# Performance work log

Measured on AMD Instinct MI355X. Metric: run time of the kernel, lower is better.

Reference implementation:

```python
import jax, jax.numpy as jnp
import numpy as np

N = 20000   # nodes
E = 320000  # edges
F0 = 32     # num_features
H = 8       # GAT heads
G = 64      # graphs in batch


def setup_inputs() -> dict:
    key = jax.random.key(0)
    ks = jax.random.split(key, 16)
    def p(k, shape, s=0.05):
        return jax.random.normal(k, shape, jnp.float32) * s
    d = {}
    d['x'] = jax.random.normal(ks[0], (N, F0), jnp.float32)
    d['edge_index'] = jax.random.randint(ks[1], (2, E), 0, N, dtype=jnp.int32)
    d['edge_weights'] = jax.random.uniform(ks[2], (E,), jnp.float32)
    d['batch'] = jnp.sort(jax.random.randint(ks[3], (N,), 0, G, dtype=jnp.int32))
    # GATConv(32 -> 32, heads=8)
    d['W_gat'] = p(ks[4], (F0, H * F0)); d['att_src'] = p(ks[5], (H, F0))
    d['att_dst'] = p(ks[6], (H, F0));    d['b_gat'] = jnp.zeros((H * F0,), jnp.float32)
    # residual Linear(256 -> 1024) (widened so the residual add is shape-consistent)
    d['W_res'] = p(ks[7], (H * F0, 1024)); d['b_res'] = jnp.zeros((1024,), jnp.float32)
    # GCNConv(256 -> 512) + BN1
    d['W2'] = p(ks[8], (H * F0, 512)); d['b2'] = jnp.zeros((512,), jnp.float32)
    d['g1'] = jnp.ones((512,), jnp.float32); d['be1'] = jnp.zeros((512,), jnp.float32)
    d['m1'] = jnp.zeros((512,), jnp.float32); d['v1'] = jnp.ones((512,), jnp.float32)
    # GCNConv(512 -> 1024) + BN2
    d['W3'] = p(ks[9], (512, 1024)); d['b3'] = jnp.zeros((1024,), jnp.float32)
    d['g2'] = jnp.ones((1024,), jnp.float32); d['be2'] = jnp.zeros((1024,), jnp.float32)
    d['m2'] = jnp.zeros((1024,), jnp.float32); d['v2'] = jnp.ones((1024,), jnp.float32)
    # head
    d['Wf1'] = p(ks[10], (1024, 256)); d['bf1'] = jnp.zeros((256,), jnp.float32)
    d['Wf2'] = p(ks[11], (256, 2));    d['bf2'] = jnp.zeros((2,), jnp.float32)
    return d


def _add_self_loops(edge_index, edge_weight, n):
    loop = jnp.arange(n, dtype=edge_index.dtype)
    ei = jnp.concatenate([edge_index, jnp.stack([loop, loop])], axis=1)
    ew = jnp.concatenate([edge_weight, jnp.ones((n,), edge_weight.dtype)])
    return ei, ew


def _gat(x, edge_index, W, att_src, att_dst, b, n):
    # PyG GATConv, concat=True, eval (attention dropout off). Self-loops already added.
    src, dst = edge_index[0], edge_index[1]
    h = (x @ W).reshape(n, H, -1)                    # [N,H,C]
    a_s = jnp.einsum('nhc,hc->nh', h, att_src)        # [N,H]
    a_d = jnp.einsum('nhc,hc->nh', h, att_dst)
    e = jax.nn.leaky_relu(a_s[src] + a_d[dst], 0.2)   # [E,H]
    m = jax.ops.segment_max(e, dst, num_segments=n)   # softmax over incoming edges
    ex = jnp.exp(e - m[dst])
    s = jax.ops.segment_sum(ex, dst, num_segments=n)
    alpha = ex / s[dst]
    out = jax.ops.segment_sum(h[src] * alpha[:, :, None], dst, num_segments=n)
    return out.reshape(n, -1) + b                     # [N,H*C]


def _gcn(x, edge_index, w, W, b, n):
    # PyG GCNConv with symmetric normalization; self-loops (weight 1) already added.
    src, dst = edge_index[0], edge_index[1]
    deg = jax.ops.segment_sum(w, dst, num_segments=n)
    dinv = jnp.where(deg > 0, jax.lax.rsqrt(jnp.maximum(deg, 1e-12)), 0.0)
    norm = dinv[src] * w * dinv[dst]                  # [E]
    h = x @ W                                         # transform first (cheaper)
    return jax.ops.segment_sum(h[src] * norm[:, None], dst, num_segments=n) + b


def _bn(x, g, b, m, v):
    return g * (x - m) * jax.lax.rsqrt(v + 1e-5) + b


def reference(x, edge_index, edge_weights, batch, W_gat, att_src, att_dst, b_gat,
              W_res, b_res, W2, b2, g1, be1, m1, v1, W3, b3, g2, be2, m2, v2,
              Wf1, bf1, Wf2, bf2):
    n = x.shape[0]
    ei, ew = _add_self_loops(edge_index, edge_weights, n)
    h = jax.nn.relu(_gat(x, ei, W_gat, att_src, att_dst, b_gat, n))   # [N,256]
    res = h @ W_res + b_res                                           # [N,1024]
    h = _gcn(h, ei, ew, W2, b2, n)                                    # [N,512]
    h = jax.nn.relu(_bn(h, g1, be1, m1, v1))
    h = _gcn(h, ei, ew, W3, b3, n)                                    # [N,1024]
    h = jax.nn.relu(_bn(h, g2, be2, m2, v2))
    h = h + res
    pooled = jax.ops.segment_max(h, batch, num_segments=G)            # global max pool [G,1024]
    z = jax.nn.relu(pooled @ Wf1 + bf1)                               # dropout is eval no-op
    return z @ Wf2 + bf2                                              # [G,2]
```

## Files before the change

kernel.cpp:

```cpp
#include <hip/hip_runtime.h>
#include <hip/hip_bf16.h>

#define NN 20000
#define EE 320000
#define GG 64
#define EN (EE + NN)
#define MT 157
#define SB 79

typedef float f32x4 __attribute__((ext_vector_type(4)));
typedef __bf16 bf16x4 __attribute__((ext_vector_type(4)));
typedef __bf16 bf16x8 __attribute__((ext_vector_type(8)));

__device__ __forceinline__ void gl_lds16(const void* g, void* l) {
    __builtin_amdgcn_global_load_lds((const __attribute__((address_space(1))) void*)g,
                                     (__attribute__((address_space(3))) void*)l, 16, 0, 0);
}

__global__ void sentinel_kernel(float* out, int n) {
    int i = blockIdx.x * 256 + threadIdx.x;
    if (i < n) out[i] = 12345.0f;
}

__global__ void init_kernel(int* deg_cnt, float* deg_w, int* fill, float* pooled) {
    int i = blockIdx.x * 256 + threadIdx.x;
    if (i < NN) { deg_cnt[i] = 1; deg_w[i] = 1.0f; fill[i] = 0; }
    if (i < GG * 1024) pooled[i] = -INFINITY;
}

__global__ void deg_kernel(const int* __restrict__ ei, const float* __restrict__ ew,
                           int* deg_cnt, float* deg_w) {
    int e = blockIdx.x * 256 + threadIdx.x;
    if (e >= EE) return;
    int dst = ei[EE + e];
    atomicAdd(&deg_cnt[dst], 1);
    atomicAdd(&deg_w[dst], ew[e]);
}

__global__ __launch_bounds__(256) void scan_blocks(const int* __restrict__ deg_cnt, int* __restrict__ bsum) {
    __shared__ int red[256];
    int tid = threadIdx.x, i = blockIdx.x * 256 + tid;
    red[tid] = (i < NN) ? deg_cnt[i] : 0;
    __syncthreads();
    for (int s = 128; s > 0; s >>= 1) { if (tid < s) red[tid] += red[tid + s]; __syncthreads(); }
    if (tid == 0) bsum[blockIdx.x] = red[0];
}

__global__ __launch_bounds__(256) void scan_write(const int* __restrict__ deg_cnt,
                                                  const int* __restrict__ bsum, int* __restrict__ rowptr) {
    __shared__ int sc[256];
    __shared__ int red[256];
    int tid = threadIdx.x, b = blockIdx.x, i = b * 256 + tid;
    red[tid] = (tid < b && tid < SB) ? bsum[tid] : 0;
    __syncthreads();
    for (int s = 128; s > 0; s >>= 1) { if (tid < s) red[tid] += red[tid + s]; __syncthreads(); }
    int boff = red[0];
    __syncthreads();
    int v = (i < NN) ? deg_cnt[i] : 0;
    sc[tid] = v;
    __syncthreads();
    for (int ofs = 1; ofs < 256; ofs <<= 1) {
        int t = (tid >= ofs) ? sc[tid - ofs] : 0;
        __syncthreads();
        sc[tid] += t;
        __syncthreads();
    }
    if (i < NN) rowptr[i] = boff + sc[tid] - v;
    if (b == SB - 1 && tid == 255) rowptr[NN] = boff + sc[255];
}

__global__ void fill_kernel(const int* __restrict__ ei, const float* __restrict__ ew,
                            const float* __restrict__ deg_w, const int* __restrict__ rowptr,
                            int* fill, int2* __restrict__ csre) {
    int e = blockIdx.x * 256 + threadIdx.x;
    if (e >= EN) return;
    int src, dst; float w;
    if (e < EE) { src = ei[e]; dst = ei[EE + e]; w = ew[e]; }
    else        { src = dst = e - EE; w = 1.0f; }
    int pos = atomicAdd(&fill[dst], 1);
    int slot = rowptr[dst] + pos;
    float norm = rsqrtf(deg_w[src]) * w * rsqrtf(deg_w[dst]);
    csre[slot] = make_int2(src, __float_as_int(norm));
}

__global__ __launch_bounds__(256) void convert_all(
    const float* __restrict__ W2, const float* __restrict__ W3, const float* __restrict__ Wres,
    __bf16* __restrict__ W2t, __bf16* __restrict__ W3t, __bf16* __restrict__ Wrt)
{
    __shared__ float tile[64][65];
    int b = blockIdx.x;
    const float* W; __bf16* Wt; int K, N, bx, by;
    if (b < 32)       { W = W2;   Wt = W2t; K = 256; N = 512;  int bb = b;       bx = bb & 7;  by = bb >> 3; }
    else if (b < 160) { W = W3;   Wt = W3t; K = 512; N = 1024; int bb = b - 32;  bx = bb & 15; by = bb >> 4; }
    else              { W = Wres; Wt = Wrt; K = 256; N = 1024; int bb = b - 160; bx = bb & 15; by = bb >> 4; }
    int kb = by * 64, nb = bx * 64;
    int tx = threadIdx.x & 63, ty = threadIdx.x >> 6;
#pragma unroll
    for (int i = ty; i < 64; i += 4)
        tile[i][tx] = W[(size_t)(kb + i) * N + nb + tx];
    __syncthreads();
#pragma unroll
    for (int i = ty; i < 64; i += 4)
        Wt[(size_t)(nb + i) * K + kb + tx] = (__bf16)tile[tx][i];
}


__global__ __launch_bounds__(256) void a_compute(
    const float* __restrict__ x, const float* __restrict__ W,
    const float* __restrict__ att_s, const float* __restrict__ att_d,
    float* __restrict__ a_s, float* __restrict__ a_d)
{
    __shared__ float wss[8][32], wsd[8][32];
    __shared__ float xs[32][33];
    int tid = threadIdx.x;
    {
        int h = tid >> 5, k = tid & 31;
        float s = 0.f, d = 0.f;
#pragma unroll
        for (int c = 0; c < 32; c++) {
            float wv = W[k * 256 + h * 32 + c];
            s += wv * att_s[h * 32 + c];
            d += wv * att_d[h * 32 + c];
        }
        wss[h][k] = s; wsd[h][k] = d;
    }
    __syncthreads();
    for (int n0 = blockIdx.x * 32; n0 < NN; n0 += gridDim.x * 32) {
#pragma unroll
        for (int i = 0; i < 4; i++) {
            int idx = tid + i * 256;
            xs[idx >> 5][idx & 31] = x[(size_t)n0 * 32 + idx];
        }
        __syncthreads();
        int nl = tid >> 3, h = tid & 7;
        float s = 0.f, d = 0.f;
#pragma unroll
        for (int k = 0; k < 32; k++) {
            float xv = xs[nl][k];
            s += xv * wss[h][k];
            d += xv * wsd[h][k];
        }
        a_s[(n0 + nl) * 8 + h] = s;
        a_d[(n0 + nl) * 8 + h] = d;
        __syncthreads();
    }
}

__global__ __launch_bounds__(256) void gat_agg_x(
    const int* __restrict__ rowptr, const int2* __restrict__ csre,
    const float* __restrict__ a_s, const float* __restrict__ a_d,
    const float* __restrict__ x, __bf16* __restrict__ xagg)
{
    int widx = threadIdx.x >> 6, lane = threadIdx.x & 63;
    int node = blockIdx.x * 4 + widx;
    int base = rowptr[node], deg = rowptr[node + 1] - base;
    int hA = lane & 7, eslot = lane >> 3;
    int c = lane & 31, half = lane >> 5;
    float adA = a_d[node * 8 + hA];
    float acc0[4] = {}, acc1[4] = {}, acc2[4] = {}, acc3[4] = {};

    if (deg <= 64) {
        int sv = (lane < deg) ? csre[base + lane].x : 0;
        float ev[8];
        float psum = 0.f;
#pragma unroll
        for (int j = 0; j < 8; j++) {
            int e = j * 8 + eslot;
            float v = 0.f;
            if (e < deg) {
                int src = __shfl(sv, e);
                float t = a_s[src * 8 + hA] + adA;
                t = (t > 0.f) ? t : 0.2f * t;
                v = __expf(t);
            }
            ev[j] = v;
            psum += v;
        }
#pragma unroll
        for (int m = 8; m <= 32; m <<= 1) psum += __shfl_xor(psum, m);
        float sinv[4];
#pragma unroll
        for (int jj = 0; jj < 4; jj++) sinv[jj] = 1.f / __shfl(psum, half * 4 + jj);
#pragma unroll
        for (int j = 0; j < 8; j++) {
            if (j * 8 >= deg) break;
            int lim = min(8, deg - j * 8);
            int t = 0;
            for (; t + 3 < lim; t += 4) {
                int sA = __shfl(sv, j * 8 + t),     sB = __shfl(sv, j * 8 + t + 1);
                int sC = __shfl(sv, j * 8 + t + 2), sD = __shfl(sv, j * 8 + t + 3);
                float xvA = x[(size_t)sA * 32 + c];
                float xvB = x[(size_t)sB * 32 + c];
                float xvC = x[(size_t)sC * 32 + c];
                float xvD = x[(size_t)sD * 32 + c];
#pragma unroll
                for (int jj = 0; jj < 4; jj++) {
                    int hb = half * 4 + jj;
                    acc0[jj] += __shfl(ev[j], (t << 3) | hb) * sinv[jj] * xvA;
                    acc1[jj] += __shfl(ev[j], ((t + 1) << 3) | hb) * sinv[jj] * xvB;
                    acc2[jj] += __shfl(ev[j], ((t + 2) << 3) | hb) * sinv[jj] * xvC;
                    acc3[jj] += __shfl(ev[j], ((t + 3) << 3) | hb) * sinv[jj] * xvD;
                }
            }
            for (; t < lim; t++) {
                int src = __shfl(sv, j * 8 + t);
                float xv = x[(size_t)src * 32 + c];
#pragma unroll
                for (int jj = 0; jj < 4; jj++) {
                    float a = __shfl(ev[j], (t << 3) | (half * 4 + jj)) * sinv[jj];
                    acc0[jj] += a * xv;
                }
            }
        }
    } else {
        float sum = 0.f;
        for (int e = 0; e < deg; e++) {
            int src = csre[base + e].x;
            float t = a_s[src * 8 + hA] + adA;
            t = (t > 0.f) ? t : 0.2f * t;
            sum += __expf(t);
        }
        float sinv[4], ad4[4];
#pragma unroll
        for (int jj = 0; jj < 4; jj++) {
            sinv[jj] = 1.f / __shfl(sum, half * 4 + jj);
            ad4[jj] = a_d[node * 8 + half * 4 + jj];
        }
        for (int e = 0; e < deg; e++) {
            int src = csre[base + e].x;
            float xv = x[(size_t)src * 32 + c];
#pragma unroll
            for (int jj = 0; jj < 4; jj++) {
                float t = a_s[src * 8 + half * 4 + jj] + ad4[jj];
                t = (t > 0.f) ? t : 0.2f * t;
                acc0[jj] += __expf(t) * sinv[jj] * xv;
            }
        }
    }
#pragma unroll
    for (int jj = 0; jj < 4; jj++)
        xagg[(size_t)node * 256 + (half * 4 + jj) * 32 + c] =
            (__bf16)((acc0[jj] + acc1[jj]) + (acc2[jj] + acc3[jj]));
}

__global__ __launch_bounds__(256) void gat_post(
    const __bf16* __restrict__ xagg, const float* __restrict__ W,
    const float* __restrict__ b_gat, __bf16* __restrict__ h1)
{
    __shared__ float Ws[32 * 256];
    int tid = threadIdx.x;
#pragma unroll
    for (int k = 0; k < 32; k++) Ws[k * 256 + tid] = W[k * 256 + tid];
    float bg = b_gat[tid];
    int lbase = tid & 32;
    __syncthreads();
    for (int n = blockIdx.x; n < NN; n += gridDim.x) {
        float xv = (float)xagg[(size_t)n * 256 + tid];
        float acc = 0.f;
#pragma unroll
        for (int k = 0; k < 32; k++) acc += __shfl(xv, lbase + k) * Ws[k * 256 + tid];
        h1[(size_t)n * 256 + tid] = (__bf16)fmaxf(acc + bg, 0.f);
    }
}

template <int C, int SPLIT>
__global__ __launch_bounds__(256) void gcn_agg(
    const int* __restrict__ rowptr, const int2* __restrict__ csre,
    const __bf16* __restrict__ feat, __bf16* __restrict__ out)
{
    constexpr int V = C / (64 * SPLIT);
    int widx = threadIdx.x >> 6, lane = threadIdx.x & 63;
    int node = blockIdx.x * (4 / SPLIT) + widx / SPLIT;
    int half = widx % SPLIT;
    int coff = half * (C / SPLIT) + lane * V;
    int base = rowptr[node], deg = rowptr[node + 1] - base;
    float acc0[V], acc1[V], acc2[V], acc3[V];
#pragma unroll
    for (int j = 0; j < V; j++) { acc0[j] = 0.f; acc1[j] = 0.f; acc2[j] = 0.f; acc3[j] = 0.f; }
    const __bf16* fb = feat + coff;
    typedef __bf16 bf16v __attribute__((ext_vector_type(V)));
    for (int e0 = 0; e0 < deg; e0 += 64) {
        int cnt = min(64, deg - e0);
        int sv = 0; float wv = 0.f;
        if (lane < cnt) { int2 m = csre[base + e0 + lane]; sv = m.x; wv = __int_as_float(m.y); }
        int s = 0;
        for (; s + 3 < cnt; s += 4) {
            int sA = __shfl(sv, s),     sB = __shfl(sv, s + 1);
            int sC = __shfl(sv, s + 2), sD = __shfl(sv, s + 3);
            float wA = __shfl(wv, s),     wB = __shfl(wv, s + 1);
            float wC = __shfl(wv, s + 2), wD = __shfl(wv, s + 3);
            bf16v fA = *(const bf16v*)(fb + (size_t)sA * C);
            bf16v fB = *(const bf16v*)(fb + (size_t)sB * C);
            bf16v fC = *(const bf16v*)(fb + (size_t)sC * C);
            bf16v fD = *(const bf16v*)(fb + (size_t)sD * C);
#pragma unroll
            for (int j = 0; j < V; j++) {
                acc0[j] += wA * (float)fA[j]; acc1[j] += wB * (float)fB[j];
                acc2[j] += wC * (float)fC[j]; acc3[j] += wD * (float)fD[j];
            }
        }
        for (; s < cnt; s++) {
            int src = __shfl(sv, s);
            float w = __shfl(wv, s);
            bf16v f = *(const bf16v*)(fb + (size_t)src * C);
#pragma unroll
            for (int j = 0; j < V; j++) acc0[j] += w * (float)f[j];
        }
    }
    bf16v o;
#pragma unroll
    for (int j = 0; j < V; j++) o[j] = (__bf16)((acc0[j] + acc1[j]) + (acc2[j] + acc3[j]));
    *(bf16v*)(out + (size_t)node * C + coff) = o;
}


__device__ __forceinline__ void stage_async64(
    const __bf16* __restrict__ A, int K, const __bf16* __restrict__ Wt,
    int bm, int bn, int k0, int tid, __bf16* As, __bf16* Bs)
{
#pragma unroll
    for (int i = 0; i < 2; i++) {
        int j = i * 512 + tid;
        int r = j >> 3, c = j & 7;
        const __bf16* gp = A + (size_t)(bm + r) * K + k0 + ((c ^ (r & 7)) * 8);
        gl_lds16(gp, As + (size_t)(j & ~63) * 8);
    }
#pragma unroll
    for (int i = 0; i < 2; i++) {
        int j = i * 512 + tid;
        int r = j >> 3, c = j & 7;
        const __bf16* gp = Wt + (size_t)(bn + r) * K + k0 + ((c ^ (r & 7)) * 8);
        gl_lds16(gp, Bs + (size_t)(j & ~63) * 8);
    }
}

__device__ __forceinline__ void mfma_step64(
    const __bf16* As, const __bf16* Bs, int wr, int wc, int l16, int q, f32x4 (&acc)[4][2])
{
#pragma unroll
    for (int ks = 0; ks < 2; ks++) {
        bf16x8 af[4], bfv[2];
#pragma unroll
        for (int mt = 0; mt < 4; mt++) {
            int row = wr * 64 + mt * 16 + l16;
            af[mt] = *(const bf16x8*)(As + row * 64 + (((ks * 4 + q) ^ (row & 7)) * 8));
        }
#pragma unroll
        for (int nt = 0; nt < 2; nt++) {
            int row = wc * 32 + nt * 16 + l16;
            bfv[nt] = *(const bf16x8*)(Bs + row * 64 + (((ks * 4 + q) ^ (row & 7)) * 8));
        }
#pragma unroll
        for (int mt = 0; mt < 4; mt++)
#pragma unroll
            for (int nt = 0; nt < 2; nt++)
                acc[mt][nt] = __builtin_amdgcn_mfma_f32_16x16x32_bf16(af[mt], bfv[nt], acc[mt][nt], 0, 0, 0);
    }
}

__device__ __forceinline__ void gemm_loop(
    const __bf16* __restrict__ A, int K, const __bf16* __restrict__ Wt,
    int bm, int bn, int tid, int wr, int wc, int l16, int q,
    __bf16* As, __bf16* Bs, f32x4 (&acc)[4][2])
{
    for (int k0 = 0; k0 < K; k0 += 64) {
        stage_async64(A, K, Wt, bm, bn, k0, tid, As, Bs);
        __syncthreads();
        mfma_step64(As, Bs, wr, wc, l16, q, acc);
        __syncthreads();
    }
}

__global__ __launch_bounds__(512) void gemm_bn_relu(
    const __bf16* __restrict__ A, const __bf16* __restrict__ Wt,
    int M, int K, int Nc,
    const float* __restrict__ bias,
    const float* __restrict__ g, const float* __restrict__ be,
    const float* __restrict__ mu, const float* __restrict__ var,
    __bf16* __restrict__ C)
{
    __shared__ __bf16 As[128 * 64];
    __shared__ __bf16 Bs[128 * 64];
    int tid = threadIdx.x;
    int w = tid >> 6, wr = w >> 2, wc = w & 3;
    int l = tid & 63, q = l >> 4, l16 = l & 15;
    int i = blockIdx.x;
    int k = (i & 3) * MT + (i >> 2);
    int bm = (k >> 2) * 128, bn = (k & 3) * 128;
    f32x4 acc[4][2] = {};
    gemm_loop(A, K, Wt, bm, bn, tid, wr, wc, l16, q, As, Bs, acc);
#pragma unroll
    for (int nt = 0; nt < 2; nt++) {
        int gn = bn + wc * 32 + nt * 16 + l16;
        float s = g[gn] * rsqrtf(var[gn] + 1e-5f);
        float t = be[gn] - mu[gn] * s;
        float bv = bias[gn];
#pragma unroll
        for (int mt = 0; mt < 4; mt++)
#pragma unroll
            for (int r = 0; r < 4; r++) {
                int gm = bm + wr * 64 + mt * 16 + q * 4 + r;
                if (gm < M) C[(size_t)gm * Nc + gn] = (__bf16)fmaxf((acc[mt][nt][r] + bv) * s + t, 0.f);
            }
    }
}

__device__ __forceinline__ void atomicMaxFloat(float* addr, float value) {
    if (value >= 0.f) atomicMax((int*)addr, __float_as_int(value));
    else              atomicMin((unsigned int*)addr, __float_as_uint(value));
}

__global__ __launch_bounds__(512) void gemm_final(
    const __bf16* __restrict__ A1, const __bf16* __restrict__ W3t,
    const __bf16* __restrict__ A2, const __bf16* __restrict__ Wrt,
    const float* __restrict__ b3, const float* __restrict__ bres,
    const float* __restrict__ g, const float* __restrict__ be,
    const float* __restrict__ mu, const float* __restrict__ var,
    const int* __restrict__ batch, float* __restrict__ pooled)
{
    const int M = NN;
    __shared__ __bf16 As[128 * 64];
    __shared__ __bf16 Bs[128 * 64];
    __shared__ int bat[128];
    int tid = threadIdx.x;
    int w = tid >> 6, wr = w >> 2, wc = w & 3;
    int l = tid & 63, q = l >> 4, l16 = l & 15;
    int i = blockIdx.x;
    int k = (i & 7) * MT + (i >> 3);
    int bm = (k >> 3) * 128, bn = (k & 7) * 128;
    if (tid < 128) bat[tid] = (bm + tid < M) ? batch[bm + tid] : -1;
    f32x4 acc[4][2] = {};
    f32x4 accR[4][2] = {};
    gemm_loop(A1, 512, W3t, bm, bn, tid, wr, wc, l16, q, As, Bs, acc);
    gemm_loop(A2, 256, Wrt, bm, bn, tid, wr, wc, l16, q, As, Bs, accR);
#pragma unroll
    for (int nt = 0; nt < 2; nt++) {
        int gn = bn + wc * 32 + nt * 16 + l16;
        float s = g[gn] * rsqrtf(var[gn] + 1e-5f);
        float t = be[gn] - mu[gn] * s;
        float bv3 = b3[gn];
        float bvr = bres[gn];
        int cb = -1; float run = 0.f;
#pragma unroll
        for (int mt = 0; mt < 4; mt++)
#pragma unroll
            for (int r = 0; r < 4; r++) {
                int lr = wr * 64 + mt * 16 + q * 4 + r;
                int id = bat[lr];
                if (id < 0) continue;
                float v = fmaxf((acc[mt][nt][r] + bv3) * s + t, 0.f) + accR[mt][nt][r] + bvr;
                if (id == cb) run = fmaxf(run, v);
                else {
                    if (cb >= 0) atomicMaxFloat(&pooled[cb * 1024 + gn], run);
                    cb = id; run = v;
                }
            }
        if (cb >= 0) atomicMaxFloat(&pooled[cb * 1024 + gn], run);
    }
}

__global__ void head_kernel(
    const float* __restrict__ pooled, const float* __restrict__ Wf1, const float* __restrict__ bf1,
    const float* __restrict__ Wf2, const float* __restrict__ bf2, float* __restrict__ out)
{
    int gph = blockIdx.x, tid = threadIdx.x;
    __shared__ float prow[1024];
    __shared__ float zred[256];
    for (int i = tid; i < 1024; i += 256) prow[i] = pooled[gph * 1024 + i];
    __syncthreads();
    float z = 0.f;
    for (int k = 0; k < 1024; k++) z += prow[k] * Wf1[k * 256 + tid];
    z = fmaxf(z + bf1[tid], 0.f);
    for (int c = 0; c < 2; c++) {
        zred[tid] = z * Wf2[tid * 2 + c];
        __syncthreads();
        for (int s = 128; s > 0; s >>= 1) { if (tid < s) zred[tid] += zred[tid + s]; __syncthreads(); }
        if (tid == 0) out[gph * 2 + c] = zred[0] + bf2[c];
        __syncthreads();
    }
}

extern "C" void kernel_launch(void* const* d_in, const int* in_sizes, int n_in,
                              void* d_out, int out_size, void* d_ws, size_t ws_size,
                              hipStream_t stream) {
    const float* x       = (const float*)d_in[0];
    const int*   ei      = (const int*)d_in[1];
    const float* ew      = (const float*)d_in[2];
    const int*   batch   = (const int*)d_in[3];
    const float* W_gat   = (const float*)d_in[4];
    const float* att_src = (const float*)d_in[5];
    const float* att_dst = (const float*)d_in[6];
    const float* b_gat   = (const float*)d_in[7];
    const float* W_res   = (const float*)d_in[8];
    const float* b_res   = (const float*)d_in[9];
    const float* W2      = (const float*)d_in[10];
    const float* b2v     = (const float*)d_in[11];
    const float* g1      = (const float*)d_in[12];
    const float* be1     = (const float*)d_in[13];
    const float* m1      = (const float*)d_in[14];
    const float* v1      = (const float*)d_in[15];
    const float* W3      = (const float*)d_in[16];
    const float* b3      = (const float*)d_in[17];
    const float* g2      = (const float*)d_in[18];
    const float* be2     = (const float*)d_in[19];
    const float* m2      = (const float*)d_in[20];
    const float* v2      = (const float*)d_in[21];
    const float* Wf1     = (const float*)d_in[22];
    const float* bf1     = (const float*)d_in[23];
    const float* Wf2     = (const float*)d_in[24];
    const float* bf2v    = (const float*)d_in[25];
    float* out           = (float*)d_out;

    char* ws = (char*)d_ws;
    size_t off = 0;
    auto alloc = [&](size_t bytes) { size_t o = off; off += (bytes + 255) & ~(size_t)255; return o; };
    size_t o_hlin   = alloc((size_t)NN * 256 * 2);
    size_t o_h1     = alloc((size_t)NN * 256 * 2);
    size_t o_h2     = alloc((size_t)NN * 512 * 2);
    size_t o_agg2   = alloc((size_t)NN * 512 * 2);
    size_t o_as     = alloc((size_t)NN * 8 * 4);
    size_t o_ad     = alloc((size_t)NN * 8 * 4);
    size_t o_degc   = alloc((size_t)NN * 4);
    size_t o_degw   = alloc((size_t)NN * 4);
    size_t o_rowptr = alloc((size_t)(NN + 1) * 4);
    size_t o_fill   = alloc((size_t)NN * 4);
    size_t o_bsum   = alloc((size_t)SB * 4);
    size_t o_csre   = alloc((size_t)EN * 8);
    size_t o_pool   = alloc((size_t)GG * 1024 * 4);
    size_t o_w2t    = alloc((size_t)512 * 256 * 2);
    size_t o_w3t    = alloc((size_t)1024 * 512 * 2);
    size_t o_wrt    = alloc((size_t)1024 * 256 * 2);
    if (off > ws_size) {
        sentinel_kernel<<<(out_size + 255) / 256, 256, 0, stream>>>(out, out_size);
        return;
    }

    __bf16* xagg   = (__bf16*)(ws + o_hlin);
    __bf16* agg1   = xagg;
    __bf16* h1     = (__bf16*)(ws + o_h1);
    __bf16* h2     = (__bf16*)(ws + o_h2);
    __bf16* agg2   = (__bf16*)(ws + o_agg2);
    float*  a_s    = (float*)(ws + o_as);
    float*  a_d    = (float*)(ws + o_ad);
    int*    degc   = (int*)(ws + o_degc);
    float*  degw   = (float*)(ws + o_degw);
    int*    rowptr = (int*)(ws + o_rowptr);
    int*    fillb  = (int*)(ws + o_fill);
    int*    bsum   = (int*)(ws + o_bsum);
    int2*   csre   = (int2*)(ws + o_csre);
    float*  pooled = (float*)(ws + o_pool);
    __bf16* W2t    = (__bf16*)(ws + o_w2t);
    __bf16* W3t    = (__bf16*)(ws + o_w3t);
    __bf16* Wrt    = (__bf16*)(ws + o_wrt);

    convert_all<<<224, 256, 0, stream>>>(W2, W3, W_res, W2t, W3t, Wrt);
    a_compute<<<128, 256, 0, stream>>>(x, W_gat, att_src, att_dst, a_s, a_d);

    init_kernel<<<256, 256, 0, stream>>>(degc, degw, fillb, pooled);
    deg_kernel<<<(EE + 255) / 256, 256, 0, stream>>>(ei, ew, degc, degw);
    scan_blocks<<<SB, 256, 0, stream>>>(degc, bsum);
    scan_write<<<SB, 256, 0, stream>>>(degc, bsum, rowptr);
    fill_kernel<<<(EN + 255) / 256, 256, 0, stream>>>(ei, ew, degw, rowptr, fillb, csre);

    gat_agg_x<<<NN / 4, 256, 0, stream>>>(rowptr, csre, a_s, a_d, x, xagg);
    gat_post<<<1280, 256, 0, stream>>>(xagg, W_gat, b_gat, h1);

    gcn_agg<256, 1><<<NN / 4, 256, 0, stream>>>(rowptr, csre, h1, agg1);
    gemm_bn_relu<<<4 * MT, 512, 0, stream>>>(agg1, W2t, NN, 256, 512, b2v,
        g1, be1, m1, v1, h2);
    gcn_agg<512, 2><<<NN / 2, 256, 0, stream>>>(rowptr, csre, h2, agg2);
    gemm_final<<<8 * MT, 512, 0, stream>>>(agg2, W3t, h1, Wrt,
        b3, b_res, g2, be2, m2, v2, batch, pooled);

    head_kernel<<<GG, 256, 0, stream>>>(pooled, Wf1, bf1, Wf2, bf2v, out);
}
```

Baseline: 404.7 us.

## Double-buffer LDS tiles in the MFMA GEMMs to overlap loads with compute

Replaces the single-buffer load/sync/compute/sync GEMM loop with a two-stage ping-pong LDS pipeline. The next K-tile is fetched with async global-to-LDS loads while MFMAs run on the current tile, leaving one barrier per step. In the final GEMM the W3 and residual GEMMs are merged into one 12-step pipelined loop. Per-block LDS doubles, which may lower the number of blocks resident per CU.

```diff
diff --git a/kernel.cpp b/kernel.cpp
--- a/kernel.cpp
+++ b/kernel.cpp
@@ -314,6 +314,8 @@
 }
 
 
+#define TBUF (128 * 64)
+
 __device__ __forceinline__ void stage_async64(
     const __bf16* __restrict__ A, int K, const __bf16* __restrict__ Wt,
     int bm, int bn, int k0, int tid, __bf16* As, __bf16* Bs)
@@ -358,16 +360,25 @@
     }
 }
 
-__device__ __forceinline__ void gemm_loop(
+__device__ __forceinline__ void gemm_loop_pipe(
     const __bf16* __restrict__ A, int K, const __bf16* __restrict__ Wt,
     int bm, int bn, int tid, int wr, int wc, int l16, int q,
     __bf16* As, __bf16* Bs, f32x4 (&acc)[4][2])
 {
-    for (int k0 = 0; k0 < K; k0 += 64) {
-        stage_async64(A, K, Wt, bm, bn, k0, tid, As, Bs);
-        __syncthreads();
-        mfma_step64(As, Bs, wr, wc, l16, q, acc);
-        __syncthreads();
+    int NT = K >> 6;
+    stage_async64(A, K, Wt, bm, bn, 0, tid, As, Bs);
+    asm volatile("s_waitcnt vmcnt(0) lgkmcnt(0)" ::: "memory");
+    __builtin_amdgcn_s_barrier();
+    int cur = 0;
+    for (int t = 0; t < NT; ++t) {
+        if (t + 1 < NT)
+            stage_async64(A, K, Wt, bm, bn, (t + 1) * 64, tid, As + (cur ^ 1) * TBUF, Bs + (cur ^ 1) * TBUF);
+        mfma_step64(As + cur * TBUF, Bs + cur * TBUF, wr, wc, l16, q, acc);
+        if (t + 1 < NT) {
+            asm volatile("s_waitcnt vmcnt(0)" ::: "memory");
+            __builtin_amdgcn_s_barrier();
+        }
+        cur ^= 1;
     }
 }
 
@@ -379,8 +390,8 @@
     const float* __restrict__ mu, const float* __restrict__ var,
     __bf16* __restrict__ C)
 {
-    __shared__ __bf16 As[128 * 64];
-    __shared__ __bf16 Bs[128 * 64];
+    __shared__ __bf16 As[2 * TBUF];
+    __shared__ __bf16 Bs[2 * TBUF];
     int tid = threadIdx.x;
     int w = tid >> 6, wr = w >> 2, wc = w & 3;
     int l = tid & 63, q = l >> 4, l16 = l & 15;
@@ -388,7 +399,7 @@
     int k = (i & 3) * MT + (i >> 2);
     int bm = (k >> 2) * 128, bn = (k & 3) * 128;
     f32x4 acc[4][2] = {};
-    gemm_loop(A, K, Wt, bm, bn, tid, wr, wc, l16, q, As, Bs, acc);
+    gemm_loop_pipe(A, K, Wt, bm, bn, tid, wr, wc, l16, q, As, Bs, acc);
 #pragma unroll
     for (int nt = 0; nt < 2; nt++) {
         int gn = bn + wc * 32 + nt * 16 + l16;
@@ -419,8 +430,8 @@
     const int* __restrict__ batch, float* __restrict__ pooled)
 {
     const int M = NN;
-    __shared__ __bf16 As[128 * 64];
-    __shared__ __bf16 Bs[128 * 64];
+    __shared__ __bf16 As[2 * TBUF];
+    __shared__ __bf16 Bs[2 * TBUF];
     __shared__ int bat[128];
     int tid = threadIdx.x;
     int w = tid >> 6, wr = w >> 2, wc = w & 3;
@@ -431,8 +442,26 @@
     if (tid < 128) bat[tid] = (bm + tid < M) ? batch[bm + tid] : -1;
     f32x4 acc[4][2] = {};
     f32x4 accR[4][2] = {};
-    gemm_loop(A1, 512, W3t, bm, bn, tid, wr, wc, l16, q, As, Bs, acc);
-    gemm_loop(A2, 256, Wrt, bm, bn, tid, wr, wc, l16, q, As, Bs, accR);
+    stage_async64(A1, 512, W3t, bm, bn, 0, tid, As, Bs);
+    asm volatile("s_waitcnt vmcnt(0) lgkmcnt(0)" ::: "memory");
+    __builtin_amdgcn_s_barrier();
+    int cur = 0;
+    for (int s = 0; s < 12; ++s) {
+        if (s + 1 < 12) {
+            int sn = s + 1;
+            if (sn < 8) stage_async64(A1, 512, W3t, bm, bn, sn * 64, tid,
+                                      As + (cur ^ 1) * TBUF, Bs + (cur ^ 1) * TBUF);
+            else        stage_async64(A2, 256, Wrt, bm, bn, (sn - 8) * 64, tid,
+                                      As + (cur ^ 1) * TBUF, Bs + (cur ^ 1) * TBUF);
+        }
+        if (s < 8) mfma_step64(As + cur * TBUF, Bs + cur * TBUF, wr, wc, l16, q, acc);
+        else       mfma_step64(As + cur * TBUF, Bs + cur * TBUF, wr, wc, l16, q, accR);
+        if (s + 1 < 12) {
+            asm volatile("s_waitcnt vmcnt(0)" ::: "memory");
+            __builtin_amdgcn_s_barrier();
+        }
+        cur ^= 1;
+    }
 #pragma unroll
     for (int nt = 0; nt < 2; nt++) {
         int gn = bn + wc * 32 + nt * 16 + l16;
```

Result: slower. 447.5 us (+10.6%).
